# Performance work log

Hardware: AMD Instinct MI355X
Metric: run time of the kernel (lower is better)

The kernel has to match this reference:

```python
import jax, jax.numpy as jnp
import numpy as np

B, HRES, WRES, C, HEADS, WS, SS = 32, 64, 64, 256, 8, 8, 4
N = WS * WS
HID = 4 * C
EPS = 1e-5


def _rel_pos_index(ws):
    coords = np.stack(np.meshgrid(np.arange(ws), np.arange(ws), indexing='ij'))  # [2,ws,ws]
    cf = coords.reshape(2, -1)
    rel = (cf[:, :, None] - cf[:, None, :]).transpose(1, 2, 0)  # [N,N,2]
    rel[:, :, 0] += ws - 1
    rel[:, :, 1] += ws - 1
    rel[:, :, 0] *= 2 * ws - 1
    return rel.sum(-1).reshape(-1)  # [N*N]


def _attn_mask(H, W, ws, ss):
    img = np.zeros((H, W))
    cnt = 0
    for hs in (slice(0, -ws), slice(-ws, -ss), slice(-ss, None)):
        for wsl in (slice(0, -ws), slice(-ws, -ss), slice(-ss, None)):
            img[hs, wsl] = cnt
            cnt += 1
    mw = img.reshape(H // ws, ws, W // ws, ws).transpose(0, 2, 1, 3).reshape(-1, ws * ws)
    am = mw[:, None, :] - mw[:, :, None]  # [nW,N,N]
    return np.where(am != 0, -100.0, 0.0).astype(np.float32)


_RPI = jnp.asarray(_rel_pos_index(WS))
_MASK = jnp.asarray(_attn_mask(HRES, WRES, WS, SS))  # [nW,N,N]


def _ln(x, g, b):
    m = x.mean(-1, keepdims=True)
    v = ((x - m) ** 2).mean(-1, keepdims=True)
    return (x - m) / jnp.sqrt(v + EPS) * g + b


def setup_inputs() -> dict:
    key = jax.random.key(0)
    ks = jax.random.split(key, 16)
    s = 0.02
    return {
        'x': jax.random.normal(ks[0], (B, HRES * WRES, C), jnp.float32),
        'norm1_g': jnp.ones((C,), jnp.float32),
        'norm1_b': jnp.zeros((C,), jnp.float32),
        'qkv_w': jax.random.normal(ks[1], (3 * C, C), jnp.float32) * s,
        'qkv_b': jnp.zeros((3 * C,), jnp.float32),
        'rpb_table': jax.random.normal(ks[2], ((2 * WS - 1) ** 2, HEADS), jnp.float32) * s,
        'proj_w': jax.random.normal(ks[3], (C, C), jnp.float32) * s,
        'proj_b': jnp.zeros((C,), jnp.float32),
        'norm2_g': jnp.ones((C,), jnp.float32),
        'norm2_b': jnp.zeros((C,), jnp.float32),
        'fc1_w': jax.random.normal(ks[4], (HID, C), jnp.float32) * s,
        'fc1_b': jnp.zeros((HID,), jnp.float32),
        'fc2_w': jax.random.normal(ks[5], (C, HID), jnp.float32) * s,
        'fc2_b': jnp.zeros((C,), jnp.float32),
        'H': HRES,
        'W': WRES,
    }


def reference(x, norm1_g, norm1_b, qkv_w, qkv_b, rpb_table, proj_w, proj_b,
              norm2_g, norm2_b, fc1_w, fc1_b, fc2_w, fc2_b, H, W):
    Bn, L, Cd = x.shape
    ws, ss, nh = WS, SS, HEADS
    hd = Cd // nh
    shortcut = x
    h = _ln(x, norm1_g, norm1_b).reshape(Bn, H, W, Cd)
    # cyclic shift (H,W divisible by ws -> no padding needed)
    h = jnp.roll(h, (-ss, -ss), axis=(1, 2))
    # window partition: [B,H,W,C] -> [B*nW, N, C]
    h = h.reshape(Bn, H // ws, ws, W // ws, ws, Cd).transpose(0, 1, 3, 2, 4, 5).reshape(-1, N, Cd)
    qkv = (h @ qkv_w.T + qkv_b).reshape(-1, N, 3, nh, hd).transpose(2, 0, 3, 1, 4)
    q, k, v = qkv[0], qkv[1], qkv[2]  # [B_,h,N,d]
    attn = jnp.einsum('bhnd,bhmd->bhnm', q * (hd ** -0.5), k)
    rpb = rpb_table[_RPI].reshape(N, N, nh).transpose(2, 0, 1)  # [h,N,N]
    attn = attn + rpb[None]
    nW = _MASK.shape[0]
    attn = attn.reshape(Bn, nW, nh, N, N) + _MASK[None, :, None]
    attn = jax.nn.softmax(attn.reshape(-1, nh, N, N), axis=-1)
    o = jnp.einsum('bhnm,bhmd->bhnd', attn, v).transpose(0, 2, 1, 3).reshape(-1, N, Cd)
    o = o @ proj_w.T + proj_b
    # window reverse + reverse shift
    o = o.reshape(Bn, H // ws, W // ws, ws, ws, Cd).transpose(0, 1, 3, 2, 4, 5).reshape(Bn, H, W, Cd)
    o = jnp.roll(o, (ss, ss), axis=(1, 2)).reshape(Bn, L, Cd)
    x = shortcut + o
    h2 = _ln(x, norm2_g, norm2_b)
    h2 = jax.nn.gelu(h2 @ fc1_w.T + fc1_b, approximate=False)
    return x + (h2 @ fc2_w.T + fc2_b)
```

## Files before the change

kernel.cpp:

```cpp
#include <hip/hip_runtime.h>
#include <hip/hip_bf16.h>
#include <stdint.h>

typedef __bf16 bf16_t;
typedef __bf16 bf16x8 __attribute__((ext_vector_type(8)));
typedef float f32x4 __attribute__((ext_vector_type(4)));

#define MROWS 131072

__device__ __forceinline__ bf16_t to_bf16(float f) {
  __hip_bfloat16 h = __float2bfloat16(f);
  return *reinterpret_cast<bf16_t*>(&h);
}

__device__ __forceinline__ f32x4 mfma16(bf16x8 a, bf16x8 b, f32x4 c) {
  return __builtin_amdgcn_mfma_f32_16x16x32_bf16(a, b, c, 0, 0, 0);
}

__device__ __forceinline__ void gload16(const void* g, void* l) {
  __builtin_amdgcn_global_load_lds(
      (const __attribute__((address_space(1))) void*)g,
      (__attribute__((address_space(3))) void*)l, 16, 0, 0);
}

__device__ __forceinline__ int map_row(int m) {
  int b   = m >> 12;
  int rem = m & 4095;
  int win = rem >> 6;
  int n   = rem & 63;
  int gh  = ((win >> 3) << 3) + (n >> 3);
  int gw  = ((win & 7) << 3) + (n & 7);
  int sh  = (gh + 4) & 63;
  int sw  = (gw + 4) & 63;
  return (b << 12) + (sh << 6) + sw;
}

__global__ __launch_bounds__(256) void cvt_kernel(const float* __restrict__ in,
                                                  bf16_t* __restrict__ out, int n) {
  int i = blockIdx.x * 256 + threadIdx.x;
  if (i < n) out[i] = to_bf16(in[i]);
}

__global__ __launch_bounds__(256) void bias_kernel(const float* __restrict__ rpbt,
                                                   float* __restrict__ bias) {
  int idx = blockIdx.x * 256 + threadIdx.x;
  int m = idx & 63, n = (idx >> 6) & 63, h = (idx >> 12) & 7, c = idx >> 15;
  int yn = n >> 3, xn = n & 7, ym = m >> 3, xm = m & 7;
  float v = rpbt[((yn - ym + 7) * 15 + (xn - xm + 7)) * 8 + h];
  int rn = (c & 2) ? (yn < 4 ? 1 : 2) : 0;
  int cn = (c & 1) ? (xn < 4 ? 1 : 2) : 0;
  int rm = (c & 2) ? (ym < 4 ? 1 : 2) : 0;
  int cm = (c & 1) ? (xm < 4 ? 1 : 2) : 0;
  if (rn * 3 + cn != rm * 3 + cm) v -= 100.0f;
  bias[idx] = v;
}

__global__ __launch_bounds__(256) void ln_kernel(const float* __restrict__ xin,
                                                 const float* __restrict__ g,
                                                 const float* __restrict__ b,
                                                 bf16_t* __restrict__ out) {
  int row  = (blockIdx.x << 2) + (threadIdx.x >> 6);
  int lane = threadIdx.x & 63;
  float4 v = *reinterpret_cast<const float4*>(xin + (size_t)row * 256 + (lane << 2));
  float s = v.x + v.y + v.z + v.w;
#pragma unroll
  for (int d = 1; d < 64; d <<= 1) s += __shfl_xor(s, d);
  float mean = s * 0.00390625f;
  float ax = v.x - mean, ay = v.y - mean, az = v.z - mean, aw = v.w - mean;
  float s2 = ax * ax + ay * ay + az * az + aw * aw;
#pragma unroll
  for (int d = 1; d < 64; d <<= 1) s2 += __shfl_xor(s2, d);
  float rstd = rsqrtf(s2 * 0.00390625f + 1e-5f);
  float4 gv = *reinterpret_cast<const float4*>(g + (lane << 2));
  float4 bv = *reinterpret_cast<const float4*>(b + (lane << 2));
  typedef __bf16 bf16x4 __attribute__((ext_vector_type(4)));
  bf16x4 o4;
  o4[0] = to_bf16(ax * rstd * gv.x + bv.x);
  o4[1] = to_bf16(ay * rstd * gv.y + bv.y);
  o4[2] = to_bf16(az * rstd * gv.z + bv.z);
  o4[3] = to_bf16(aw * rstd * gv.w + bv.w);
  *reinterpret_cast<bf16x4*>(out + (size_t)row * 256 + (lane << 2)) = o4;
}

template <int EPI>
__global__ __launch_bounds__(256) void gemm_bt(const bf16_t* __restrict__ A,
                                               const bf16_t* __restrict__ W,
                                               const float* __restrict__ bias,
                                               void* __restrict__ outp,
                                               int M, int N, int K) {
  __shared__ __align__(16) bf16_t As[128 * 32];
  __shared__ __align__(16) bf16_t Bs[128 * 32];
  const int tid  = threadIdx.x;
  const int lane = tid & 63, lo = lane & 15, hi = lane >> 4;
  const int wave = tid >> 6;
  const int bm = blockIdx.y << 7, bn = blockIdx.x << 7;
  const int wr = (wave >> 1) << 6, wc = (wave & 1) << 6;
  f32x4 acc[4][4] = {};

  for (int k0 = 0; k0 < K; k0 += 32) {
    __syncthreads();
#pragma unroll
    for (int it = 0; it < 2; ++it) {
      int ch = (it << 8) + tid;
      int r = ch >> 2, kf = (ch & 3) << 3;
      gload16(A + (size_t)(bm + r) * K + (k0 + kf), &As[ch << 3]);
      gload16(W + (size_t)(bn + r) * K + (k0 + kf), &Bs[ch << 3]);
    }
    __syncthreads();
    bf16x8 af[4], bfr[4];
#pragma unroll
    for (int i = 0; i < 4; ++i)
      af[i] = *reinterpret_cast<const bf16x8*>(&As[(wr + (i << 4) + lo) * 32 + (hi << 3)]);
#pragma unroll
    for (int j = 0; j < 4; ++j)
      bfr[j] = *reinterpret_cast<const bf16x8*>(&Bs[(wc + (j << 4) + lo) * 32 + (hi << 3)]);
#pragma unroll
    for (int i = 0; i < 4; ++i)
#pragma unroll
      for (int j = 0; j < 4; ++j)
        acc[i][j] = mfma16(af[i], bfr[j], acc[i][j]);
  }

  float bv[4];
#pragma unroll
  for (int j = 0; j < 4; ++j) bv[j] = bias[bn + wc + (j << 4) + lo];

#pragma unroll
  for (int i = 0; i < 4; ++i) {
#pragma unroll
    for (int r = 0; r < 4; ++r) {
      int row = bm + wr + (i << 4) + (hi << 2) + r;
      if constexpr (EPI == 3) {
        float* o = (float*)outp;
#pragma unroll
        for (int j = 0; j < 4; ++j) {
          int col = bn + wc + (j << 4) + lo;
          size_t idx = (size_t)row * 256 + col;
          o[idx] = o[idx] + acc[i][j][r] + bv[j];
        }
      } else {
        bf16_t* o = (bf16_t*)outp;
#pragma unroll
        for (int j = 0; j < 4; ++j) {
          int col = bn + wc + (j << 4) + lo;
          float v = acc[i][j][r] + bv[j];
          if constexpr (EPI == 1) v = 0.5f * v * (1.0f + erff(v * 0.70710678118654752f));
          o[(size_t)row * N + col] = to_bf16(v);
        }
      }
    }
  }
}

__global__ __launch_bounds__(512, 2) void mega_attn(
    const float* __restrict__ x, const float* __restrict__ n1g,
    const float* __restrict__ n1b, const bf16_t* __restrict__ qkv_wb,
    const float* __restrict__ qkv_b, const bf16_t* __restrict__ proj_wb,
    const float* __restrict__ proj_b, const float* __restrict__ bias,
    float* __restrict__ out) {
  extern __shared__ __align__(16) char smem_raw[];
  bf16_t* Sm = (bf16_t*)smem_raw;
  bf16_t* A_lds = Sm;
  const int tid = threadIdx.x;
  const int lane = tid & 63, lo = lane & 15, hi = lane >> 4;
  const int h = tid >> 6;
  const int win = blockIdx.x;
  bf16_t* Wv    = Sm + 16896 + h * 7424;
  bf16_t* q_lds = Wv;
  bf16_t* k_lds = Wv + 2560;
  bf16_t* Vt    = Wv + 5120;
  bf16_t* Pl    = Wv;

  {
    const int row = tid >> 3, s = tid & 7;
    const int src = map_row((win << 6) + row);
    const float* xp = x + (size_t)src * 256 + (s << 5);
    float f[32];
#pragma unroll
    for (int c = 0; c < 8; ++c) {
      float4 v = *reinterpret_cast<const float4*>(xp + (c << 2));
      f[c * 4 + 0] = v.x; f[c * 4 + 1] = v.y; f[c * 4 + 2] = v.z; f[c * 4 + 3] = v.w;
    }
    float sum = 0.0f;
#pragma unroll
    for (int e = 0; e < 32; ++e) sum += f[e];
#pragma unroll
    for (int d = 1; d < 8; d <<= 1) sum += __shfl_xor(sum, d);
    float mean = sum * 0.00390625f;
    float var = 0.0f;
#pragma unroll
    for (int e = 0; e < 32; ++e) { float t = f[e] - mean; var += t * t; }
#pragma unroll
    for (int d = 1; d < 8; d <<= 1) var += __shfl_xor(var, d);
    float rstd = rsqrtf(var * 0.00390625f + 1e-5f);
    const float* gp = n1g + (s << 5);
    const float* bp = n1b + (s << 5);
#pragma unroll
    for (int c = 0; c < 4; ++c) {
      bf16x8 w;
#pragma unroll
      for (int e = 0; e < 8; ++e) {
        int idx = (c << 3) + e;
        w[e] = to_bf16((f[idx] - mean) * rstd * gp[idx] + bp[idx]);
      }
      *reinterpret_cast<bf16x8*>(&A_lds[row * 264 + (s << 5) + (c << 3)]) = w;
    }
  }
  __syncthreads();

  f32x4 aq[2][4] = {}, ak[2][4] = {}, av[2][4] = {};
#pragma unroll 2
  for (int kk = 0; kk < 8; ++kk) {
    const int k0 = kk << 5;
    bf16x8 fb[4];
#pragma unroll
    for (int j = 0; j < 4; ++j)
      fb[j] = *reinterpret_cast<const bf16x8*>(&A_lds[((j << 4) + lo) * 264 + k0 + (hi << 3)]);
    bf16x8 wfq[2], wfk[2], wfv[2];
#pragma unroll
    for (int i = 0; i < 2; ++i) {
      int drow = h * 32 + (i << 4) + lo;
      wfq[i] = *reinterpret_cast<const bf16x8*>(qkv_wb + (size_t)(drow      ) * 256 + k0 + (hi << 3));
      wfk[i] = *reinterpret_cast<const bf16x8*>(qkv_wb + (size_t)(drow + 256) * 256 + k0 + (hi << 3));
      wfv[i] = *reinterpret_cast<const bf16x8*>(qkv_wb + (size_t)(drow + 512) * 256 + k0 + (hi << 3));
    }
#pragma unroll
    for (int i = 0; i < 2; ++i)
#pragma unroll
      for (int j = 0; j < 4; ++j) {
        aq[i][j] = mfma16(wfq[i], fb[j], aq[i][j]);
        ak[i][j] = mfma16(wfk[i], fb[j], ak[i][j]);
        av[i][j] = mfma16(wfv[i], fb[j], av[i][j]);
      }
  }

#pragma unroll
  for (int i = 0; i < 2; ++i)
#pragma unroll
    for (int r = 0; r < 4; ++r) {
      int d = (i << 4) + (hi << 2) + r;
      float bq = qkv_b[h * 32 + d];
      float bk = qkv_b[256 + h * 32 + d];
      float bv = qkv_b[512 + h * 32 + d];
#pragma unroll
      for (int j = 0; j < 4; ++j) {
        int n = (j << 4) + lo;
        q_lds[n * 40 + d] = to_bf16(aq[i][j][r] + bq);
        k_lds[n * 40 + d] = to_bf16(ak[i][j][r] + bk);
        Vt[d * 72 + n]    = to_bf16(av[i][j][r] + bv);
      }
    }

  bf16x8 qa[4], ka[4];
#pragma unroll
  for (int i = 0; i < 4; ++i)
    qa[i] = *reinterpret_cast<const bf16x8*>(&q_lds[((i << 4) + lo) * 40 + (hi << 3)]);
#pragma unroll
  for (int j = 0; j < 4; ++j)
    ka[j] = *reinterpret_cast<const bf16x8*>(&k_lds[((j << 4) + lo) * 40 + (hi << 3)]);
  f32x4 s4[4][4] = {};
#pragma unroll
  for (int i = 0; i < 4; ++i)
#pragma unroll
    for (int j = 0; j < 4; ++j) s4[i][j] = mfma16(qa[i], ka[j], s4[i][j]);

  const int wh = (win & 63) >> 3, ww = win & 7;
  const int cls = ((wh == 7) ? 2 : 0) + ((ww == 7) ? 1 : 0);
  const float* bb = bias + ((size_t)cls * 8 + h) * 4096;
  const float scale = 0.17677669529663687f;

  float pinv[4][4];
#pragma unroll
  for (int i = 0; i < 4; ++i) {
#pragma unroll
    for (int r = 0; r < 4; ++r) {
      int n = (i << 4) + (hi << 2) + r;
      const float* brow = bb + n * 64 + lo;
      float vals[4], mx = -1e30f;
#pragma unroll
      for (int j = 0; j < 4; ++j) {
        float val = s4[i][j][r] * scale + brow[j << 4];
        vals[j] = val;
        mx = fmaxf(mx, val);
      }
#pragma unroll
      for (int d = 1; d < 16; d <<= 1) mx = fmaxf(mx, __shfl_xor(mx, d));
      float sum = 0.0f;
#pragma unroll
      for (int j = 0; j < 4; ++j) {
        float p = __expf(vals[j] - mx);
        sum += p;
        Pl[n * 72 + (j << 4) + lo] = to_bf16(p);
      }
#pragma unroll
      for (int d = 1; d < 16; d <<= 1) sum += __shfl_xor(sum, d);
      pinv[i][r] = 1.0f / sum;
    }
  }

  f32x4 oa[4][2] = {};
#pragma unroll
  for (int kt = 0; kt < 2; ++kt) {
    bf16x8 pa[4], va[2];
#pragma unroll
    for (int i = 0; i < 4; ++i)
      pa[i] = *reinterpret_cast<const bf16x8*>(&Pl[((i << 4) + lo) * 72 + (kt << 5) + (hi << 3)]);
#pragma unroll
    for (int dt = 0; dt < 2; ++dt)
      va[dt] = *reinterpret_cast<const bf16x8*>(&Vt[((dt << 4) + lo) * 72 + (kt << 5) + (hi << 3)]);
#pragma unroll
    for (int i = 0; i < 4; ++i)
#pragma unroll
      for (int dt = 0; dt < 2; ++dt) oa[i][dt] = mfma16(pa[i], va[dt], oa[i][dt]);
  }

  __syncthreads();
#pragma unroll
  for (int i = 0; i < 4; ++i)
#pragma unroll
    for (int r = 0; r < 4; ++r) {
      int n = (i << 4) + (hi << 2) + r;
      float piv = pinv[i][r];
#pragma unroll
      for (int dt = 0; dt < 2; ++dt)
        A_lds[n * 264 + h * 32 + (dt << 4) + lo] = to_bf16(oa[i][dt][r] * piv);
    }
  __syncthreads();

  f32x4 ap[4][2] = {};
#pragma unroll 2
  for (int kk = 0; kk < 8; ++kk) {
    const int k0 = kk << 5;
    bf16x8 fa[4], wp[2];
#pragma unroll
    for (int i = 0; i < 4; ++i)
      fa[i] = *reinterpret_cast<const bf16x8*>(&A_lds[((i << 4) + lo) * 264 + k0 + (hi << 3)]);
#pragma unroll
    for (int jj = 0; jj < 2; ++jj)
      wp[jj] = *reinterpret_cast<const bf16x8*>(proj_wb + (size_t)(h * 32 + (jj << 4) + lo) * 256 + k0 + (hi << 3));
#pragma unroll
    for (int i = 0; i < 4; ++i)
#pragma unroll
      for (int jj = 0; jj < 2; ++jj)
        ap[i][jj] = mfma16(fa[i], wp[jj], ap[i][jj]);
  }
#pragma unroll
  for (int i = 0; i < 4; ++i)
#pragma unroll
    for (int r = 0; r < 4; ++r) {
      int m = (i << 4) + (hi << 2) + r;
      int xr = map_row((win << 6) + m);
#pragma unroll
      for (int jj = 0; jj < 2; ++jj) {
        int col = h * 32 + (jj << 4) + lo;
        size_t idx = (size_t)xr * 256 + col;
        out[idx] = x[idx] + ap[i][jj][r] + proj_b[col];
      }
    }
}

extern "C" void kernel_launch(void* const* d_in, const int* in_sizes, int n_in,
                              void* d_out, int out_size, void* d_ws, size_t ws_size,
                              hipStream_t stream) {
  const float* x      = (const float*)d_in[0];
  const float* n1g    = (const float*)d_in[1];
  const float* n1b    = (const float*)d_in[2];
  const float* qkv_w  = (const float*)d_in[3];
  const float* qkv_b  = (const float*)d_in[4];
  const float* rpbt   = (const float*)d_in[5];
  const float* proj_w = (const float*)d_in[6];
  const float* proj_b = (const float*)d_in[7];
  const float* n2g    = (const float*)d_in[8];
  const float* n2b    = (const float*)d_in[9];
  const float* fc1_w  = (const float*)d_in[10];
  const float* fc1_b  = (const float*)d_in[11];
  const float* fc2_w  = (const float*)d_in[12];
  const float* fc2_b  = (const float*)d_in[13];
  float* out = (float*)d_out;
  char*  ws  = (char*)d_ws;

  const size_t MB64 = 67108864;
  bf16_t* h2   = (bf16_t*)(ws);
  bf16_t* x2n  = (bf16_t*)(ws + MB64);
  bf16_t* wb   = (bf16_t*)(ws + 2 * MB64);
  bf16_t* qkv_wb  = wb;
  bf16_t* proj_wb = qkv_wb + 196608;
  bf16_t* fc1_wb  = proj_wb + 65536;
  bf16_t* fc2_wb  = fc1_wb + 262144;
  float*  biast   = (float*)(fc2_wb + 262144);

  static const int MEGA_LDS = 152576;
  hipFuncSetAttribute(reinterpret_cast<const void*>(mega_attn),
                      hipFuncAttributeMaxDynamicSharedMemorySize, MEGA_LDS);

  cvt_kernel<<<768, 256, 0, stream>>>(qkv_w, qkv_wb, 196608);
  cvt_kernel<<<256, 256, 0, stream>>>(proj_w, proj_wb, 65536);
  cvt_kernel<<<1024, 256, 0, stream>>>(fc1_w, fc1_wb, 262144);
  cvt_kernel<<<1024, 256, 0, stream>>>(fc2_w, fc2_wb, 262144);
  bias_kernel<<<512, 256, 0, stream>>>(rpbt, biast);

  mega_attn<<<2048, 512, MEGA_LDS, stream>>>(x, n1g, n1b, qkv_wb, qkv_b,
                                             proj_wb, proj_b, biast, out);

  ln_kernel<<<32768, 256, 0, stream>>>(out, n2g, n2b, x2n);

  for (int c = 0; c < 4; ++c) {
    const bf16_t* xa = x2n + (size_t)c * 32768 * 256;
    gemm_bt<1><<<dim3(8, 256), 256, 0, stream>>>(xa, fc1_wb, fc1_b, h2, 32768, 1024, 256);
    gemm_bt<3><<<dim3(2, 256), 256, 0, stream>>>(h2, fc2_wb, fc2_b, out + (size_t)c * 32768 * 256,
                                                 32768, 256, 1024);
  }
}
```

Baseline: 644.4 us.

## Split each attention head across two waves with 1024-thread blocks

Doubles the mega_attn block from 512 to 1024 threads so that two waves share each head. The work is split this way: the QKV projection by output-dim halves, the scores, softmax and PV by query-row halves, and the output projection by 16-column slices per wave. LayerNorm row processing is spread over 16 lanes per row instead of 8. Extra __syncthreads are added because the two waves of a head share the q/k/P LDS buffers. The goal is more waves in flight per CU to hide latency, since the LDS footprint already limits the kernel to one block per CU. The cost is more barriers, and the tighter launch bound may cut the register budget or cause spills.

```diff
diff --git a/kernel.cpp b/kernel.cpp
--- a/kernel.cpp
+++ b/kernel.cpp
@@ -152,7 +152,7 @@
   }
 }
 
-__global__ __launch_bounds__(512, 2) void mega_attn(
+__global__ __launch_bounds__(1024, 4) void mega_attn(
     const float* __restrict__ x, const float* __restrict__ n1g,
     const float* __restrict__ n1b, const bf16_t* __restrict__ qkv_wb,
     const float* __restrict__ qkv_b, const bf16_t* __restrict__ proj_wb,
@@ -163,7 +163,8 @@
   bf16_t* A_lds = Sm;
   const int tid = threadIdx.x;
   const int lane = tid & 63, lo = lane & 15, hi = lane >> 4;
-  const int h = tid >> 6;
+  const int wave = tid >> 6;
+  const int h = wave >> 1, sub = wave & 1;
   const int win = blockIdx.x;
   bf16_t* Wv    = Sm + 16896 + h * 7424;
   bf16_t* q_lds = Wv;
@@ -172,114 +173,111 @@
   bf16_t* Pl    = Wv;
 
   {
-    const int row = tid >> 3, s = tid & 7;
+    const int row = tid >> 4, s = tid & 15;
     const int src = map_row((win << 6) + row);
-    const float* xp = x + (size_t)src * 256 + (s << 5);
-    float f[32];
-#pragma unroll
-    for (int c = 0; c < 8; ++c) {
+    const float* xp = x + (size_t)src * 256 + (s << 4);
+    float f[16];
+#pragma unroll
+    for (int c = 0; c < 4; ++c) {
       float4 v = *reinterpret_cast<const float4*>(xp + (c << 2));
       f[c * 4 + 0] = v.x; f[c * 4 + 1] = v.y; f[c * 4 + 2] = v.z; f[c * 4 + 3] = v.w;
     }
     float sum = 0.0f;
 #pragma unroll
-    for (int e = 0; e < 32; ++e) sum += f[e];
-#pragma unroll
-    for (int d = 1; d < 8; d <<= 1) sum += __shfl_xor(sum, d);
+    for (int e = 0; e < 16; ++e) sum += f[e];
+#pragma unroll
+    for (int d = 1; d < 16; d <<= 1) sum += __shfl_xor(sum, d);
     float mean = sum * 0.00390625f;
     float var = 0.0f;
 #pragma unroll
-    for (int e = 0; e < 32; ++e) { float t = f[e] - mean; var += t * t; }
-#pragma unroll
-    for (int d = 1; d < 8; d <<= 1) var += __shfl_xor(var, d);
+    for (int e = 0; e < 16; ++e) { float t = f[e] - mean; var += t * t; }
+#pragma unroll
+    for (int d = 1; d < 16; d <<= 1) var += __shfl_xor(var, d);
     float rstd = rsqrtf(var * 0.00390625f + 1e-5f);
-    const float* gp = n1g + (s << 5);
-    const float* bp = n1b + (s << 5);
-#pragma unroll
-    for (int c = 0; c < 4; ++c) {
+    const float* gp = n1g + (s << 4);
+    const float* bp = n1b + (s << 4);
+#pragma unroll
+    for (int c = 0; c < 2; ++c) {
       bf16x8 w;
 #pragma unroll
       for (int e = 0; e < 8; ++e) {
         int idx = (c << 3) + e;
         w[e] = to_bf16((f[idx] - mean) * rstd * gp[idx] + bp[idx]);
       }
-      *reinterpret_cast<bf16x8*>(&A_lds[row * 264 + (s << 5) + (c << 3)]) = w;
+      *reinterpret_cast<bf16x8*>(&A_lds[row * 264 + (s << 4) + (c << 3)]) = w;
     }
   }
   __syncthreads();
 
-  f32x4 aq[2][4] = {}, ak[2][4] = {}, av[2][4] = {};
+  f32x4 aq[4] = {}, ak[4] = {}, av[4] = {};
+  {
+    const int drow = h * 32 + sub * 16 + lo;
 #pragma unroll 2
-  for (int kk = 0; kk < 8; ++kk) {
-    const int k0 = kk << 5;
-    bf16x8 fb[4];
-#pragma unroll
-    for (int j = 0; j < 4; ++j)
-      fb[j] = *reinterpret_cast<const bf16x8*>(&A_lds[((j << 4) + lo) * 264 + k0 + (hi << 3)]);
-    bf16x8 wfq[2], wfk[2], wfv[2];
-#pragma unroll
-    for (int i = 0; i < 2; ++i) {
-      int drow = h * 32 + (i << 4) + lo;
-      wfq[i] = *reinterpret_cast<const bf16x8*>(qkv_wb + (size_t)(drow      ) * 256 + k0 + (hi << 3));
-      wfk[i] = *reinterpret_cast<const bf16x8*>(qkv_wb + (size_t)(drow + 256) * 256 + k0 + (hi << 3));
-      wfv[i] = *reinterpret_cast<const bf16x8*>(qkv_wb + (size_t)(drow + 512) * 256 + k0 + (hi << 3));
-    }
-#pragma unroll
-    for (int i = 0; i < 2; ++i)
+    for (int kk = 0; kk < 8; ++kk) {
+      const int k0 = kk << 5;
+      bf16x8 fb[4];
+#pragma unroll
+      for (int j = 0; j < 4; ++j)
+        fb[j] = *reinterpret_cast<const bf16x8*>(&A_lds[((j << 4) + lo) * 264 + k0 + (hi << 3)]);
+      bf16x8 wfq = *reinterpret_cast<const bf16x8*>(qkv_wb + (size_t)(drow      ) * 256 + k0 + (hi << 3));
+      bf16x8 wfk = *reinterpret_cast<const bf16x8*>(qkv_wb + (size_t)(drow + 256) * 256 + k0 + (hi << 3));
+      bf16x8 wfv = *reinterpret_cast<const bf16x8*>(qkv_wb + (size_t)(drow + 512) * 256 + k0 + (hi << 3));
 #pragma unroll
       for (int j = 0; j < 4; ++j) {
-        aq[i][j] = mfma16(wfq[i], fb[j], aq[i][j]);
-        ak[i][j] = mfma16(wfk[i], fb[j], ak[i][j]);
-        av[i][j] = mfma16(wfv[i], fb[j], av[i][j]);
-      }
-  }
-
-#pragma unroll
-  for (int i = 0; i < 2; ++i)
-#pragma unroll
-    for (int r = 0; r < 4; ++r) {
-      int d = (i << 4) + (hi << 2) + r;
-      float bq = qkv_b[h * 32 + d];
-      float bk = qkv_b[256 + h * 32 + d];
-      float bv = qkv_b[512 + h * 32 + d];
-#pragma unroll
-      for (int j = 0; j < 4; ++j) {
-        int n = (j << 4) + lo;
-        q_lds[n * 40 + d] = to_bf16(aq[i][j][r] + bq);
-        k_lds[n * 40 + d] = to_bf16(ak[i][j][r] + bk);
-        Vt[d * 72 + n]    = to_bf16(av[i][j][r] + bv);
-      }
-    }
-
-  bf16x8 qa[4], ka[4];
-#pragma unroll
-  for (int i = 0; i < 4; ++i)
-    qa[i] = *reinterpret_cast<const bf16x8*>(&q_lds[((i << 4) + lo) * 40 + (hi << 3)]);
+        aq[j] = mfma16(wfq, fb[j], aq[j]);
+        ak[j] = mfma16(wfk, fb[j], ak[j]);
+        av[j] = mfma16(wfv, fb[j], av[j]);
+      }
+    }
+  }
+
+#pragma unroll
+  for (int r = 0; r < 4; ++r) {
+    int d = sub * 16 + (hi << 2) + r;
+    float bq = qkv_b[h * 32 + d];
+    float bk = qkv_b[256 + h * 32 + d];
+    float bv = qkv_b[512 + h * 32 + d];
+#pragma unroll
+    for (int j = 0; j < 4; ++j) {
+      int n = (j << 4) + lo;
+      q_lds[n * 40 + d] = to_bf16(aq[j][r] + bq);
+      k_lds[n * 40 + d] = to_bf16(ak[j][r] + bk);
+      Vt[d * 72 + n]    = to_bf16(av[j][r] + bv);
+    }
+  }
+  __syncthreads();
+
+  bf16x8 qa[2], ka[4];
+#pragma unroll
+  for (int il = 0; il < 2; ++il)
+    qa[il] = *reinterpret_cast<const bf16x8*>(&q_lds[(sub * 32 + (il << 4) + lo) * 40 + (hi << 3)]);
 #pragma unroll
   for (int j = 0; j < 4; ++j)
     ka[j] = *reinterpret_cast<const bf16x8*>(&k_lds[((j << 4) + lo) * 40 + (hi << 3)]);
-  f32x4 s4[4][4] = {};
-#pragma unroll
-  for (int i = 0; i < 4; ++i)
-#pragma unroll
-    for (int j = 0; j < 4; ++j) s4[i][j] = mfma16(qa[i], ka[j], s4[i][j]);
+  f32x4 s4[2][4] = {};
+#pragma unroll
+  for (int il = 0; il < 2; ++il)
+#pragma unroll
+    for (int j = 0; j < 4; ++j) s4[il][j] = mfma16(qa[il], ka[j], s4[il][j]);
+
+  __syncthreads();
 
   const int wh = (win & 63) >> 3, ww = win & 7;
   const int cls = ((wh == 7) ? 2 : 0) + ((ww == 7) ? 1 : 0);
   const float* bb = bias + ((size_t)cls * 8 + h) * 4096;
   const float scale = 0.17677669529663687f;
 
-  float pinv[4][4];
-#pragma unroll
-  for (int i = 0; i < 4; ++i) {
+  float pinv[2][4];
+#pragma unroll
+  for (int il = 0; il < 2; ++il) {
 #pragma unroll
     for (int r = 0; r < 4; ++r) {
-      int n = (i << 4) + (hi << 2) + r;
+      int n = sub * 32 + (il << 4) + (hi << 2) + r;
       const float* brow = bb + n * 64 + lo;
       float vals[4], mx = -1e30f;
 #pragma unroll
       for (int j = 0; j < 4; ++j) {
-        float val = s4[i][j][r] * scale + brow[j << 4];
+        float val = s4[il][j][r] * scale + brow[j << 4];
         vals[j] = val;
         mx = fmaxf(mx, val);
       }
@@ -294,69 +292,63 @@
       }
 #pragma unroll
       for (int d = 1; d < 16; d <<= 1) sum += __shfl_xor(sum, d);
-      pinv[i][r] = 1.0f / sum;
-    }
-  }
-
-  f32x4 oa[4][2] = {};
+      pinv[il][r] = 1.0f / sum;
+    }
+  }
+
+  f32x4 oa[2][2] = {};
 #pragma unroll
   for (int kt = 0; kt < 2; ++kt) {
-    bf16x8 pa[4], va[2];
-#pragma unroll
-    for (int i = 0; i < 4; ++i)
-      pa[i] = *reinterpret_cast<const bf16x8*>(&Pl[((i << 4) + lo) * 72 + (kt << 5) + (hi << 3)]);
+    bf16x8 pa[2], va[2];
+#pragma unroll
+    for (int il = 0; il < 2; ++il)
+      pa[il] = *reinterpret_cast<const bf16x8*>(&Pl[(sub * 32 + (il << 4) + lo) * 72 + (kt << 5) + (hi << 3)]);
 #pragma unroll
     for (int dt = 0; dt < 2; ++dt)
       va[dt] = *reinterpret_cast<const bf16x8*>(&Vt[((dt << 4) + lo) * 72 + (kt << 5) + (hi << 3)]);
 #pragma unroll
+    for (int il = 0; il < 2; ++il)
+#pragma unroll
+      for (int dt = 0; dt < 2; ++dt) oa[il][dt] = mfma16(pa[il], va[dt], oa[il][dt]);
+  }
+
+#pragma unroll
+  for (int il = 0; il < 2; ++il)
+#pragma unroll
+    for (int r = 0; r < 4; ++r) {
+      int n = sub * 32 + (il << 4) + (hi << 2) + r;
+      float piv = pinv[il][r];
+#pragma unroll
+      for (int dt = 0; dt < 2; ++dt)
+        A_lds[n * 264 + h * 32 + (dt << 4) + lo] = to_bf16(oa[il][dt][r] * piv);
+    }
+  __syncthreads();
+
+  {
+    const int c0 = wave << 4;
+    f32x4 ap[4] = {};
+#pragma unroll 2
+    for (int kk = 0; kk < 8; ++kk) {
+      const int k0 = kk << 5;
+      bf16x8 fa[4];
+#pragma unroll
+      for (int i = 0; i < 4; ++i)
+        fa[i] = *reinterpret_cast<const bf16x8*>(&A_lds[((i << 4) + lo) * 264 + k0 + (hi << 3)]);
+      bf16x8 wp = *reinterpret_cast<const bf16x8*>(proj_wb + (size_t)(c0 + lo) * 256 + k0 + (hi << 3));
+#pragma unroll
+      for (int i = 0; i < 4; ++i) ap[i] = mfma16(fa[i], wp, ap[i]);
+    }
+    float pb = proj_b[c0 + lo];
+#pragma unroll
     for (int i = 0; i < 4; ++i)
 #pragma unroll
-      for (int dt = 0; dt < 2; ++dt) oa[i][dt] = mfma16(pa[i], va[dt], oa[i][dt]);
-  }
-
-  __syncthreads();
-#pragma unroll
-  for (int i = 0; i < 4; ++i)
-#pragma unroll
-    for (int r = 0; r < 4; ++r) {
-      int n = (i << 4) + (hi << 2) + r;
-      float piv = pinv[i][r];
-#pragma unroll
-      for (int dt = 0; dt < 2; ++dt)
-        A_lds[n * 264 + h * 32 + (dt << 4) + lo] = to_bf16(oa[i][dt][r] * piv);
-    }
-  __syncthreads();
-
-  f32x4 ap[4][2] = {};
-#pragma unroll 2
-  for (int kk = 0; kk < 8; ++kk) {
-    const int k0 = kk << 5;
-    bf16x8 fa[4], wp[2];
-#pragma unroll
-    for (int i = 0; i < 4; ++i)
-      fa[i] = *reinterpret_cast<const bf16x8*>(&A_lds[((i << 4) + lo) * 264 + k0 + (hi << 3)]);
-#pragma unroll
-    for (int jj = 0; jj < 2; ++jj)
-      wp[jj] = *reinterpret_cast<const bf16x8*>(proj_wb + (size_t)(h * 32 + (jj << 4) + lo) * 256 + k0 + (hi << 3));
-#pragma unroll
-    for (int i = 0; i < 4; ++i)
-#pragma unroll
-      for (int jj = 0; jj < 2; ++jj)
-        ap[i][jj] = mfma16(fa[i], wp[jj], ap[i][jj]);
-  }
-#pragma unroll
-  for (int i = 0; i < 4; ++i)
-#pragma unroll
-    for (int r = 0; r < 4; ++r) {
-      int m = (i << 4) + (hi << 2) + r;
-      int xr = map_row((win << 6) + m);
-#pragma unroll
-      for (int jj = 0; jj < 2; ++jj) {
-        int col = h * 32 + (jj << 4) + lo;
-        size_t idx = (size_t)xr * 256 + col;
-        out[idx] = x[idx] + ap[i][jj][r] + proj_b[col];
-      }
-    }
+      for (int r = 0; r < 4; ++r) {
+        int m = (i << 4) + (hi << 2) + r;
+        int xr = map_row((win << 6) + m);
+        size_t idx = (size_t)xr * 256 + c0 + lo;
+        out[idx] = x[idx] + ap[i][r] + pb;
+      }
+  }
 }
 
 extern "C" void kernel_launch(void* const* d_in, const int* in_sizes, int n_in,
@@ -399,8 +391,8 @@
   cvt_kernel<<<1024, 256, 0, stream>>>(fc2_w, fc2_wb, 262144);
   bias_kernel<<<512, 256, 0, stream>>>(rpbt, biast);
 
-  mega_attn<<<2048, 512, MEGA_LDS, stream>>>(x, n1g, n1b, qkv_wb, qkv_b,
-                                             proj_wb, proj_b, biast, out);
+  mega_attn<<<2048, 1024, MEGA_LDS, stream>>>(x, n1g, n1b, qkv_wb, qkv_b,
+                                              proj_wb, proj_b, biast, out);
 
   ln_kernel<<<32768, 256, 0, stream>>>(out, n2g, n2b, x2n);
 
```

Measured after the change: 617.6 us. 1.04x faster.
